# Kernel optimization log

Hardware: AMD Instinct MI355X
Metric: run time of the kernel (lower is better)

The kernel has to match this reference:

```python
import jax, jax.numpy as jnp
import numpy as np

B, S, D, H = 2, 4096, 1024, 16
HD = D // H
KCONV = 4


def _rmsnorm(x, scale, eps=1e-6):
    return x * jax.lax.rsqrt(jnp.mean(x * x, axis=-1, keepdims=True) + eps) * scale


def _l2norm(x, eps=1e-6):
    return x * jax.lax.rsqrt(jnp.sum(x * x, axis=-1, keepdims=True) + eps)


def _causal_dwconv_silu(x, w):
    # x: [B,S,D], w: [D,K] depthwise taps (tap K-1 multiplies x[t])
    k = w.shape[1]
    s = x.shape[1]
    xp = jnp.pad(x, ((0, 0), (k - 1, 0), (0, 0)))
    out = sum(xp[:, i:i + s, :] * w[:, i] for i in range(k))
    return jax.nn.silu(out)


def _p20_scan(x, decay_log, theta):
    # BLOCK_DIAGONAL_2 rotary-state linear recurrence: channels paired into
    # complex state, s_t = a * s_{t-1} + u_t with a = exp(-exp(decay_log) + i*theta).
    b, s, d = x.shape
    xc = x.reshape(b, s, d // 2, 2)
    u = jax.lax.complex(xc[..., 0], xc[..., 1])  # [B,S,D/2]
    a = jnp.exp(-jnp.exp(decay_log)) * jnp.exp(1j * theta)  # [D/2] complex, |a|<1

    def step(carry, u_t):
        st = carry * a + u_t
        return st, st

    _, ys = jax.lax.scan(step, jnp.zeros((b, d // 2), u.dtype), jnp.swapaxes(u, 0, 1))
    ys = jnp.swapaxes(ys, 0, 1)  # [B,S,D/2]
    return jnp.stack([ys.real, ys.imag], axis=-1).reshape(b, s, d)


def _gated_delta_rule(q, k, v, g, beta):
    # q,k,v: [B,S,H,Dh]; g,beta: [B,S,H]. State S: [B,H,K,V].
    scale = q.shape[-1] ** -0.5
    q = _l2norm(q)
    k = _l2norm(k)
    qt, kt, vt = (jnp.moveaxis(t, 1, 0) for t in (q, k, v))
    gt, bt = (jnp.moveaxis(t, 1, 0) for t in (g, beta))
    s0 = jnp.zeros((q.shape[0], q.shape[2], q.shape[3], v.shape[3]), v.dtype)

    def step(state, inp):
        q_t, k_t, v_t, g_t, b_t = inp
        state = state * jnp.exp(g_t)[..., None, None]
        v_err = (v_t - jnp.einsum('bhkv,bhk->bhv', state, k_t)) * b_t[..., None]
        state = state + jnp.einsum('bhk,bhv->bhkv', k_t, v_err)
        o_t = jnp.einsum('bhkv,bhk->bhv', state, q_t) * scale
        return state, o_t

    _, o = jax.lax.scan(step, s0, (qt, kt, vt, gt, bt))
    return jnp.moveaxis(o, 0, 1)  # [B,S,H,V]


def setup_inputs() -> dict:
    key = jax.random.key(0)
    ks = jax.random.split(key, 16)
    w = lambda k, shp, s=0.02: (jax.random.normal(k, shp, jnp.float32) * s)
    ctrl_out = 3 * D + 2 * H + D  # q,k,v,decay,beta,output_gate
    ctrl_b = jnp.concatenate([
        jnp.zeros((3 * D,), jnp.float32),
        jnp.full((H,), 1.5, jnp.float32),       # decay bias
        jnp.full((H,), -2.0, jnp.float32),      # beta bias
        jnp.full((D,), -1.5, jnp.float32),      # output gate bias
    ])
    # depthwise conv init: delta at last tap + small noise
    def conv_w(k):
        base = jnp.zeros((D, KCONV), jnp.float32).at[:, -1].set(1.0)
        return base + w(k, (D, KCONV), 0.02)
    return {
        'hidden': jax.random.normal(ks[0], (B, S, D), jnp.float32),
        'p20_decay_log': w(ks[1], (D // 2,), 1.0),
        'p20_theta': jax.random.uniform(ks[2], (D // 2,), jnp.float32, 0.0, 2.0 * np.pi),
        'ctrl_W': w(ks[3], (D, ctrl_out)),
        'ctrl_b': ctrl_b,
        'p20c_W': w(ks[4], (D, 3 * D), 0.001),  # 0.05-scaled init
        'qconv_w': conv_w(ks[5]),
        'kconv_w': conv_w(ks[6]),
        'vconv_w': conv_w(ks[7]),
        'mnorm_scale': jnp.ones((HD,), jnp.float32),
        'vnorm_scale': jnp.ones((D,), jnp.float32),
        'ramp_logit': jnp.full((D,), -4.595, jnp.float32),  # logit(0.01)
        'out_W': w(ks[8], (2 * D, D), 0.02),
        'out_b': jnp.zeros((D,), jnp.float32),
    }


def reference(hidden, p20_decay_log, p20_theta, ctrl_W, ctrl_b, p20c_W,
              qconv_w, kconv_w, vconv_w, mnorm_scale, vnorm_scale,
              ramp_logit, out_W, out_b):
    b, s, d = hidden.shape
    # P20 vector-state side channel
    p20_read = _p20_scan(hidden, p20_decay_log, p20_theta)
    normed_p20 = _rmsnorm(p20_read, vnorm_scale)
    p20_q, p20_k, p20_v = jnp.split(normed_p20 @ p20c_W, 3, axis=-1)
    ramp = jax.nn.sigmoid(ramp_logit)  # [D]
    # packed control projection
    ctrl = hidden @ ctrl_W + ctrl_b
    q_in, k_in, v_in, dec_in, beta_in, gate_in = jnp.split(
        ctrl, np.cumsum([d, d, d, H, H]).tolist(), axis=-1)
    # causal depthwise conv + SiLU
    q_in = _causal_dwconv_silu(q_in, qconv_w)
    k_in = _causal_dwconv_silu(k_in, kconv_w)
    v_in = _causal_dwconv_silu(v_in, vconv_w)
    # P20-conditioned heads
    queries = (q_in + ramp * p20_q).reshape(b, s, H, HD)
    keys = (k_in + ramp * p20_k).reshape(b, s, H, HD)
    values = (v_in + ramp * p20_v).reshape(b, s, H, HD)
    g = jax.nn.log_sigmoid(dec_in.astype(jnp.float32)).astype(hidden.dtype)  # [B,S,H]
    beta = jax.nn.sigmoid(beta_in)
    reads = _gated_delta_rule(queries, keys, values, g, beta)
    normed_reads = _rmsnorm(reads, mnorm_scale).reshape(b, s, d)
    fused = jnp.concatenate([normed_reads, normed_p20], axis=-1)
    projected = fused @ out_W + out_b
    return jax.nn.sigmoid(gate_in) * projected
```

## Files before the change

kernel.cpp:

```cpp
#include <hip/hip_runtime.h>
#include <hip/hip_bf16.h>
#include <stdint.h>

#define SEQ  4096
#define NH   16
#define HD   64

typedef __attribute__((ext_vector_type(8))) short bf16x8;
typedef __attribute__((ext_vector_type(4))) float f32x4;

__device__ __forceinline__ float bf2f(unsigned short u){
  union{unsigned u;float f;} v; v.u = ((unsigned)u)<<16; return v.f;
}
__device__ __forceinline__ unsigned short f2bf(float f){
  union{float f;unsigned u;} v; v.f=f;
  return (unsigned short)((v.u + 0x7fffu + ((v.u>>16)&1u))>>16);
}
__device__ __forceinline__ float sigm(float x){ return 1.f/(1.f+__expf(-x)); }
__device__ __forceinline__ f32x4 mfma16(bf16x8 a, bf16x8 b, f32x4 c){
  return __builtin_amdgcn_mfma_f32_16x16x32_bf16(a,b,c,0,0,0);
}
__device__ __forceinline__ void gll16(const void* g, void* l){
  __builtin_amdgcn_global_load_lds((const __attribute__((address_space(1))) void*)g,
                                   (__attribute__((address_space(3))) void*)l, 16, 0, 0);
}

__global__ void k_fill(float* __restrict__ p, float v, long n){
  long i = (long)blockIdx.x*blockDim.x + threadIdx.x;
  long stride = (long)gridDim.x*blockDim.x;
  for (; i<n; i+=stride) p[i] = v;
}

__global__ void k_cvt_bf16(const float* __restrict__ in, unsigned short* __restrict__ out){
  long i = ((long)blockIdx.x*256 + threadIdx.x)*4;
  float4 v = *(const float4*)(in+i);
  ushort4 o; o.x=f2bf(v.x); o.y=f2bf(v.y); o.z=f2bf(v.z); o.w=f2bf(v.w);
  *(ushort4*)(out+i) = o;
}

__global__ void k_transpose(const float* __restrict__ in, unsigned short* __restrict__ out,
                            int R, int Cin, int Cpad){
  __shared__ float t[32][33];
  int cb = blockIdx.x*32, rb = blockIdx.y*32;
  int tx = threadIdx.x & 31, ty = threadIdx.x >> 5;
  for (int k=0;k<32;k+=8){
    int r = rb+ty+k, c = cb+tx;
    t[ty+k][tx] = (c<Cin) ? in[(long)r*Cin + c] : 0.f;
  }
  __syncthreads();
  for (int k=0;k<32;k+=8){
    int c = cb+ty+k, r = rb+tx;
    if (c<Cpad) out[(long)c*R + r] = f2bf(t[tx][ty+k]);
  }
}

#define FOR16(F) F(0,0) F(0,1) F(0,2) F(0,3) F(1,0) F(1,1) F(1,2) F(1,3) \
                 F(2,0) F(2,1) F(2,2) F(2,3) F(3,0) F(3,1) F(3,2) F(3,3)
#define FOR4(F) F(0) F(1) F(2) F(3)
#define ACC(i,j) Ac##i##j

#define GEMM_CORE(A_,lda_,Bt_,ldb_,K_)                                         \
  __shared__ unsigned short Ab[3][4096];                                       \
  __shared__ unsigned short Bb[3][4096];                                       \
  const int tid=threadIdx.x, wid=tid>>6, l=tid&63;                             \
  const int nbx=(int)gridDim.x;                                               \
  const int nwg=nbx*(int)gridDim.y;                                           \
  int flat=(int)blockIdx.y*nbx+(int)blockIdx.x;                                \
  flat=(flat&7)*(nwg>>3)+(flat>>3);                                           \
  const long m0=(long)(flat/nbx)*128, n0=(long)(flat%nbx)*128;                 \
  const int nk=(K_)>>5;                                                        \
  const int wm=(wid>>1)*64, wn=(wid&1)*64;                                     \
  const int srow0 = tid>>2;                                                    \
  const int schunk = (((tid&3) ^ ((tid>>4)&3))<<3);                            \
  const unsigned short* gA0 = (A_) + (m0+srow0)*(lda_) + schunk;               \
  const unsigned short* gA1 = (A_) + (m0+64+srow0)*(lda_) + schunk;            \
  const unsigned short* gB0 = (Bt_) + (n0+srow0)*(ldb_) + schunk;              \
  const unsigned short* gB1 = (Bt_) + (n0+64+srow0)*(ldb_) + schunk;           \
  const int ldst0 = tid*16, ldst1 = 4096 + tid*16;                             \
  f32x4 Ac00={0.f,0.f,0.f,0.f};                                                \
  f32x4 Ac01=Ac00,Ac02=Ac00,Ac03=Ac00,Ac10=Ac00,Ac11=Ac00,Ac12=Ac00,           \
        Ac13=Ac00,Ac20=Ac00,Ac21=Ac00,Ac22=Ac00,Ac23=Ac00,Ac30=Ac00,           \
        Ac31=Ac00,Ac32=Ac00,Ac33=Ac00;                                         \
  gll16(gA0, (char*)&Ab[0][0]+ldst0); gll16(gA1, (char*)&Ab[0][0]+ldst1);      \
  gll16(gB0, (char*)&Bb[0][0]+ldst0); gll16(gB1, (char*)&Bb[0][0]+ldst1);      \
  gA0+=32; gA1+=32; gB0+=32; gB1+=32;                                          \
  gll16(gA0, (char*)&Ab[1][0]+ldst0); gll16(gA1, (char*)&Ab[1][0]+ldst1);      \
  gll16(gB0, (char*)&Bb[1][0]+ldst0); gll16(gB1, (char*)&Bb[1][0]+ldst1);      \
  gA0+=32; gA1+=32; gB0+=32; gB1+=32;                                          \
  int rb=0, sb=2;                                                              \
  const int sxor = ((l>>2)&3)<<4;                                              \
  const int rao0 = (wm+(l&15))*64 + (((l>>4)<<4) ^ sxor);                      \
  const int rbo0 = (wn+(l&15))*64 + (((l>>4)<<4) ^ sxor);                      \
  for (int kt=0; kt<nk; ++kt){                                                 \
    if (kt+1<nk) { asm volatile("s_waitcnt vmcnt(4)" ::: "memory"); }          \
    else         { asm volatile("s_waitcnt vmcnt(0)" ::: "memory"); }          \
    __builtin_amdgcn_sched_barrier(0);                                         \
    __builtin_amdgcn_s_barrier();                                              \
    __builtin_amdgcn_sched_barrier(0);                                         \
    if (kt+2<nk){                                                              \
      gll16(gA0, (char*)&Ab[sb][0]+ldst0); gll16(gA1, (char*)&Ab[sb][0]+ldst1);\
      gll16(gB0, (char*)&Bb[sb][0]+ldst0); gll16(gB1, (char*)&Bb[sb][0]+ldst1);\
      gA0+=32; gA1+=32; gB0+=32; gB1+=32;                                      \
    }                                                                          \
    const char* Apt=(const char*)&Ab[rb][0];                                   \
    const char* Bpt=(const char*)&Bb[rb][0];                                   \
    bf16x8 af0=*(const bf16x8*)(Apt+rao0);      bf16x8 bf0=*(const bf16x8*)(Bpt+rbo0);      \
    bf16x8 af1=*(const bf16x8*)(Apt+rao0+1024); bf16x8 bf1=*(const bf16x8*)(Bpt+rbo0+1024); \
    bf16x8 af2=*(const bf16x8*)(Apt+rao0+2048); bf16x8 bf2=*(const bf16x8*)(Bpt+rbo0+2048); \
    bf16x8 af3=*(const bf16x8*)(Apt+rao0+3072); bf16x8 bf3=*(const bf16x8*)(Bpt+rbo0+3072); \
    __builtin_amdgcn_s_setprio(1);                                             \
    Ac00=mfma16(af0,bf0,Ac00); Ac01=mfma16(af0,bf1,Ac01);                      \
    Ac02=mfma16(af0,bf2,Ac02); Ac03=mfma16(af0,bf3,Ac03);                      \
    Ac10=mfma16(af1,bf0,Ac10); Ac11=mfma16(af1,bf1,Ac11);                      \
    Ac12=mfma16(af1,bf2,Ac12); Ac13=mfma16(af1,bf3,Ac13);                      \
    Ac20=mfma16(af2,bf0,Ac20); Ac21=mfma16(af2,bf1,Ac21);                      \
    Ac22=mfma16(af2,bf2,Ac22); Ac23=mfma16(af2,bf3,Ac23);                      \
    Ac30=mfma16(af3,bf0,Ac30); Ac31=mfma16(af3,bf1,Ac31);                      \
    Ac32=mfma16(af3,bf2,Ac32); Ac33=mfma16(af3,bf3,Ac33);                      \
    __builtin_amdgcn_s_setprio(0);                                             \
    rb = (rb==2)?0:rb+1; sb = (sb==2)?0:sb+1;                                  \
  }

__global__ __launch_bounds__(256,2) void k_gemm(
  const unsigned short* __restrict__ A, int lda,
  const unsigned short* __restrict__ Bt, int ldb,
  unsigned short* Cb, float* Cf, int ldc,
  int K, int Nvalid,
  const float* __restrict__ bias,
  const unsigned short* __restrict__ gate, int gld)
{
  GEMM_CORE(A, lda, Bt, ldb, K)
#define EPI_GEN(mi,ni) {                                                       \
  const int gn=(int)n0+wn+ni*16+(l&15);                                        \
  if (gn<Nvalid){                                                              \
    _Pragma("unroll") for(int r=0;r<4;r++){                                    \
      const long gm=m0+wm+mi*16+((l>>4)<<2)+r;                                 \
      float v=ACC(mi,ni)[r];                                                   \
      if(bias) v+=bias[gn];                                                    \
      if(gate) v*=bf2f(gate[gm*gld+gn]);                                       \
      if(Cb) Cb[gm*ldc+gn]=f2bf(v); else Cf[gm*ldc+gn]=v; } } }
  FOR16(EPI_GEN)
#undef EPI_GEN
}

__global__ __launch_bounds__(256,2) void k_gemm_ctrl(
  const unsigned short* __restrict__ A, int lda,
  const unsigned short* __restrict__ Bt, int ldb,
  unsigned short* __restrict__ ctrl,
  float* __restrict__ gbuf, float* __restrict__ bbuf,
  unsigned short* __restrict__ gateb,
  const float* __restrict__ bias)
{
  GEMM_CORE(A, lda, Bt, ldb, 1024)
#define EPI_CTRL(mi,ni) {                                                      \
  const int gn=(int)n0+wn+ni*16+(l&15);                                        \
  if (gn<4128){                                                                \
    const float bs=bias[gn];                                                   \
    _Pragma("unroll") for(int r=0;r<4;r++){                                    \
      const long gm=m0+wm+mi*16+((l>>4)<<2)+r;                                 \
      float v=ACC(mi,ni)[r]+bs;                                                \
      if (gn<3072)      ctrl[gm*3072+gn]=f2bf(v);                              \
      else if (gn<3088) gbuf[gm*16+(gn-3072)]=                                 \
                          (v>=0.f)?-log1pf(__expf(-v)):(v-log1pf(__expf(v)));  \
      else if (gn<3104) bbuf[gm*16+(gn-3088)]=sigm(v);                         \
      else              gateb[gm*1024+(gn-3104)]=f2bf(sigm(v)); } } }
  FOR16(EPI_CTRL)
#undef EPI_CTRL
}

__global__ __launch_bounds__(256,2) void k_gemm_qkv(
  const unsigned short* __restrict__ A, int lda,
  const unsigned short* __restrict__ Bt, int ldb,
  const float* __restrict__ ramp,
  unsigned short* __restrict__ Qb, unsigned short* __restrict__ Kb,
  unsigned short* __restrict__ Vb)
{
  GEMM_CORE(A, lda, Bt, ldb, 1024)
  const int seg = (int)((n0 + wn) >> 10);
  unsigned short* Ob = (seg==0)?Qb:((seg==1)?Kb:Vb);
  const int dc0=((int)n0+wn+0*16+(l&15))&1023; const float sr0=sigm(ramp[dc0]);
  const int dc1=((int)n0+wn+1*16+(l&15))&1023; const float sr1=sigm(ramp[dc1]);
  const int dc2=((int)n0+wn+2*16+(l&15))&1023; const float sr2=sigm(ramp[dc2]);
  const int dc3=((int)n0+wn+3*16+(l&15))&1023; const float sr3=sigm(ramp[dc3]);
#define EPI_QKV(mi) {                                                          \
  _Pragma("unroll") for(int r=0;r<4;r++){                                      \
    const long gm=m0+wm+mi*16+((l>>4)<<2)+r;                                   \
    float v0=bf2f(Ob[gm*1024+dc0])+sr0*ACC(mi,0)[r];                           \
    float v1=bf2f(Ob[gm*1024+dc1])+sr1*ACC(mi,1)[r];                           \
    float v2=bf2f(Ob[gm*1024+dc2])+sr2*ACC(mi,2)[r];                           \
    float v3=bf2f(Ob[gm*1024+dc3])+sr3*ACC(mi,3)[r];                           \
    if (seg<2){                                                                \
      float ss=v0*v0+v1*v1+v2*v2+v3*v3;                                        \
      ss+=__shfl_xor(ss,1); ss+=__shfl_xor(ss,2);                              \
      ss+=__shfl_xor(ss,4); ss+=__shfl_xor(ss,8);                              \
      float rs=rsqrtf(ss+1e-6f); v0*=rs; v1*=rs; v2*=rs; v3*=rs; }             \
    Ob[gm*1024+dc0]=f2bf(v0); Ob[gm*1024+dc1]=f2bf(v1);                        \
    Ob[gm*1024+dc2]=f2bf(v2); Ob[gm*1024+dc3]=f2bf(v3); } }
  FOR4(EPI_QKV)
#undef EPI_QKV
}

__global__ void k_scan1(const float* __restrict__ hidden, const float* __restrict__ dlog,
                        const float* __restrict__ theta, float2* __restrict__ finals){
  int idx = blockIdx.x*256 + threadIdx.x;
  int ch = idx & 511; int chunk = (idx>>9) & 63; int b = idx>>15;
  float e = __expf(dlog[ch]); float r = __expf(-e);
  float th = theta[ch]; float ar = r*__cosf(th), ai = r*__sinf(th);
  const float2* src = (const float2*)hidden + ((long)b*SEQ + chunk*64)*512 + ch;
  float sr=0.f, si=0.f;
  for (int j=0;j<64;j++){
    float2 u = src[(long)j*512];
    float nr = sr*ar - si*ai + u.x;
    si = sr*ai + si*ar + u.y; sr = nr;
  }
  finals[idx] = make_float2(sr,si);
}
__global__ void k_scan2(const float* __restrict__ dlog, const float* __restrict__ theta,
                        const float2* __restrict__ finals, float2* __restrict__ carry, int nb){
  int idx = blockIdx.x*256+threadIdx.x; if (idx>=nb*512) return;
  int ch = idx & 511, b = idx>>9;
  float e = __expf(dlog[ch]); float r64 = __expf(-64.f*e);
  float ang = fmodf(64.f*theta[ch], 6.2831853071795864f);
  float cr = r64*__cosf(ang), ci = r64*__sinf(ang);
  float pr=0.f, pi=0.f;
  for (int c=0;c<64;c++){
    long o = ((long)b*64 + c)*512 + ch;
    carry[o] = make_float2(pr,pi);
    float2 f = finals[o];
    float nr = pr*cr - pi*ci + f.x;
    pi = pr*ci + pi*cr + f.y; pr = nr;
  }
}
__global__ void k_scan3(const float* __restrict__ hidden, const float* __restrict__ dlog,
                        const float* __restrict__ theta, const float2* __restrict__ carry,
                        unsigned short* __restrict__ p20){
  int idx = blockIdx.x*256 + threadIdx.x;
  int ch = idx & 511; int chunk = (idx>>9) & 63; int b = idx>>15;
  float e = __expf(dlog[ch]); float r = __expf(-e);
  float th = theta[ch]; float ar = r*__cosf(th), ai = r*__sinf(th);
  long toff = (long)b*SEQ + chunk*64;
  const float2* src = (const float2*)hidden + toff*512 + ch;
  unsigned short* dst = p20 + toff*1024 + 2*ch;
  float2 c0 = carry[idx];
  float sr=c0.x, si=c0.y;
  for (int j=0;j<64;j++){
    float2 u = src[(long)j*512];
    float nr = sr*ar - si*ai + u.x;
    si = sr*ai + si*ar + u.y; sr = nr;
    ushort2 o; o.x=f2bf(sr); o.y=f2bf(si);
    *(ushort2*)(dst + (long)j*1024) = o;
  }
}

__global__ __launch_bounds__(256) void k_rms_p20(const unsigned short* __restrict__ p20,
                        const float* __restrict__ vns, unsigned short* __restrict__ fused){
  long t = blockIdx.x;
  int d = threadIdx.x*4;
  ushort4 xu = *(const ushort4*)(p20 + t*1024 + d);
  float x0=bf2f(xu.x), x1=bf2f(xu.y), x2=bf2f(xu.z), x3=bf2f(xu.w);
  float ss = x0*x0 + x1*x1 + x2*x2 + x3*x3;
  for (int o=1;o<64;o<<=1) ss += __shfl_xor(ss, o);
  __shared__ float red[4];
  if ((threadIdx.x&63)==0) red[threadIdx.x>>6] = ss;
  __syncthreads();
  ss = red[0]+red[1]+red[2]+red[3];
  float rs = rsqrtf(ss*(1.f/1024.f) + 1e-6f);
  float4 s4 = *(const float4*)(vns + d);
  ushort4 o4;
  o4.x = f2bf(x0*rs*s4.x); o4.y = f2bf(x1*rs*s4.y);
  o4.z = f2bf(x2*rs*s4.z); o4.w = f2bf(x3*rs*s4.w);
  *(ushort4*)(fused + t*2048 + 1024 + d) = o4;
}

__global__ __launch_bounds__(256) void k_conv(const unsigned short* __restrict__ ctrl,
   const float* __restrict__ qw, const float* __restrict__ kw, const float* __restrict__ vw,
   unsigned short* __restrict__ Q, unsigned short* __restrict__ Kb, unsigned short* __restrict__ Vb){
  __shared__ unsigned short pan[19][256];
  int panel = blockIdx.x;
  int tb = blockIdx.y;
  int b = tb >> 8; int s0 = (tb & 255) * 16;
  int seg = panel >> 2; int d = (panel & 3)*256 + threadIdx.x;
  int c0 = panel*256;
  long base = (long)b*SEQ*3072;
  for (int rr=0; rr<19; rr++){
    int s = s0 - 3 + rr;
    pan[rr][threadIdx.x] = (s>=0) ? ctrl[base + (long)s*3072 + c0 + threadIdx.x] : (unsigned short)0;
  }
  __syncthreads();
  const float* cw = (seg==0)?qw:((seg==1)?kw:vw);
  float w0=cw[d*4], w1=cw[d*4+1], w2=cw[d*4+2], w3=cw[d*4+3];
  unsigned short* Ob = (seg==0)?Q:((seg==1)?Kb:Vb);
  for (int tk=0; tk<16; tk++){
    long t = (long)b*SEQ + s0 + tk;
    float x = bf2f(pan[tk][threadIdx.x])*w0 + bf2f(pan[tk+1][threadIdx.x])*w1
            + bf2f(pan[tk+2][threadIdx.x])*w2 + bf2f(pan[tk+3][threadIdx.x])*w3;
    x = x * sigm(x);
    Ob[t*1024 + d] = f2bf(x);
  }
}

__global__ __launch_bounds__(64,2) void k_phase1(
    const unsigned short* __restrict__ Kg, const unsigned short* __restrict__ Vg,
    const float* __restrict__ g, const float* __restrict__ beta,
    unsigned short* __restrict__ uvT, unsigned short* __restrict__ Wrm,
    unsigned short* __restrict__ Mc, unsigned short* __restrict__ BcT){
  __shared__ unsigned short Kc[64*64];
  __shared__ unsigned short Vc[64*64];
  __shared__ float Af[64*64];
  __shared__ unsigned short uTb[64*72];
  __shared__ unsigned short wTb[64*72];
  __shared__ float Gs[64], betl[64], bgam[64], decC[64];

  int bid = blockIdx.x; int bh = bid>>6, c = bid&63;
  int blocal = bh>>4, h = bh&15;
  long t0 = (long)blocal*SEQ + c*64;
  int l = threadIdx.x;
  long cbase = (long)bid*4096;

  float G = g[(t0+l)*16 + h];
  for (int o=1;o<64;o<<=1){ float n = __shfl_up(G,o); if (l>=o) G += n; }
  float bl = beta[(t0+l)*16+h];
  Gs[l]=G; betl[l]=bl; bgam[l]=bl*__expf(G);
  float G63 = __shfl(G,63);
  decC[l] = __expf(G63 - G);
  float GamC = __expf(G63);

  for (int it=0; it<8; it++){
    int bo = it*1024 + l*16;
    int row = bo>>7, bib = bo&127;
    int sb2 = bib ^ ((row&7)<<4);
    gll16(Kg + (t0+row)*1024 + h*64 + (sb2>>1),  (char*)Kc + bo);
    gll16(Vg + (t0+row)*1024 + h*64 + (bib>>1), (char*)Vc + bo);
  }
  __syncthreads();

  bf16x8 kf[2][4];
  {
    int rr = l&15;
    #pragma unroll
    for (int t=0;t<4;t++)
      #pragma unroll
      for (int h2=0;h2<2;h2++){
        int row = t*16 + rr;
        int byt = row*128 + ((h2*64 + (l>>4)*16) ^ ((row&7)<<4));
        kf[h2][t] = *(const bf16x8*)((const char*)Kc + byt);
      }
  }
  #pragma unroll
  for (int ti=0;ti<4;ti++){
    #pragma unroll
    for (int tj=0;tj<4;tj++){
      f32x4 a = {0.f,0.f,0.f,0.f};
// ... 160 lines not shown
    short4 s4 = *(const short4*)&Sst[cbase + flat];
    *(short4*)((char*)ST + v*128 + ((2*kd0) ^ ((v&7)<<4))) = s4;
  }
  __syncthreads();

  bf16x8 qf[2][4], kfr[2][4], sf[2][4];
  #pragma unroll
  for (int t=0;t<4;t++){
    long tr = t0 + t*16 + (l&15);
    qf[0][t]  = *(const bf16x8*)(Qg + tr*1024 + h*64 + (l>>4)*8);
    qf[1][t]  = *(const bf16x8*)(Qg + tr*1024 + h*64 + 32 + (l>>4)*8);
    kfr[0][t] = *(const bf16x8*)(Kg + tr*1024 + h*64 + (l>>4)*8);
    kfr[1][t] = *(const bf16x8*)(Kg + tr*1024 + h*64 + 32 + (l>>4)*8);
    int v = t*16 + (l&15);
    sf[0][t] = *(const bf16x8*)((const char*)ST + v*128 + (((l>>4)*16) ^ ((v&7)<<4)));
    sf[1][t] = *(const bf16x8*)((const char*)ST + v*128 + ((64+(l>>4)*16) ^ ((v&7)<<4)));
  }

  f32x4 qs[4][4];
  #pragma unroll
  for (int ti=0;ti<4;ti++)
    #pragma unroll
    for (int tj=0;tj<4;tj++){
      f32x4 a = {0.f,0.f,0.f,0.f};
      a = mfma16(qf[0][ti], sf[0][tj], a);
      a = mfma16(qf[1][ti], sf[1][tj], a);
      qs[ti][tj] = a;
    }

  #pragma unroll
  for (int ti=0;ti<4;ti++)
    #pragma unroll
    for (int tj=0;tj<4;tj++){
      f32x4 a = {0.f,0.f,0.f,0.f};
      a = mfma16(qf[0][ti], kfr[0][tj], a);
      a = mfma16(qf[1][ti], kfr[1][tj], a);
      int j = tj*16 + (l&15);
      float Gj = Gs[j];
      #pragma unroll
      for (int r=0;r<4;r++){
        int i = ti*16 + ((l>>4)<<2) + r;
        float v = (j<=i)? a[r]*__expf(Gs[i]-Gj) : 0.f;
        *(unsigned short*)((char*)QKl + i*128 + ((2*j) ^ ((i&7)<<4))) = f2bf(v);
      }
    }

  #pragma unroll
  for (int ti=0; ti<4; ti++){
    int irow = ti*16 + (l&15);
    bf16x8 w0 = *(const bf16x8*)(Wrm + cbase + irow*64 + (l>>4)*8);
    bf16x8 w1 = *(const bf16x8*)(Wrm + cbase + irow*64 + 32 + (l>>4)*8);
    #pragma unroll
    for (int tj=0; tj<4; tj++){
      f32x4 a = {0.f,0.f,0.f,0.f};
      a = mfma16(w0, sf[0][tj], a);
      a = mfma16(w1, sf[1][tj], a);
      int v = tj*16 + (l&15);
      int i0 = ti*16 + ((l>>4)<<2);
      short4 uv4 = *(const short4*)(uvT + cbase + (long)v*64 + i0);
      short4 p;
      p.x=(short)f2bf(bf2f((unsigned short)uv4.x) - a[0]);
      p.y=(short)f2bf(bf2f((unsigned short)uv4.y) - a[1]);
      p.z=(short)f2bf(bf2f((unsigned short)uv4.z) - a[2]);
      p.w=(short)f2bf(bf2f((unsigned short)uv4.w) - a[3]);
      *(short4*)((char*)uT + v*128 + ((2*i0) ^ ((v&7)<<4))) = p;
    }
  }
  __syncthreads();

  float mscale[4];
  #pragma unroll
  for (int tj=0;tj<4;tj++) mscale[tj] = mns[tj*16 + (l&15)];
  #pragma unroll
  for (int ti=0; ti<4; ti++){
    int row = ti*16 + (l&15);
    bf16x8 qk0 = *(const bf16x8*)((const char*)QKl + row*128 + (((l>>4)*16) ^ ((row&7)<<4)));
    bf16x8 qk1 = *(const bf16x8*)((const char*)QKl + row*128 + ((64+(l>>4)*16) ^ ((row&7)<<4)));
    #pragma unroll
    for (int tj=0; tj<4; tj++){
      int v = tj*16 + (l&15);
      bf16x8 u0 = *(const bf16x8*)((const char*)uT + v*128 + (((l>>4)*16) ^ ((v&7)<<4)));
      bf16x8 u1 = *(const bf16x8*)((const char*)uT + v*128 + ((64+(l>>4)*16) ^ ((v&7)<<4)));
      f32x4 a;
      #pragma unroll
      for (int r=0;r<4;r++){
        float gam = __expf(Gs[ti*16 + ((l>>4)<<2) + r]);
        a[r] = qs[ti][tj][r]*gam;
      }
      a = mfma16(qk0,u0,a);
      a = mfma16(qk1,u1,a);
      qs[ti][tj] = a;
    }
  }
  #pragma unroll
  for (int ti=0; ti<4; ti++){
    #pragma unroll
    for (int r=0; r<4; r++){
      float ss = 0.f;
      #pragma unroll
      for (int tj=0;tj<4;tj++){ float v = qs[ti][tj][r]*0.125f; ss += v*v; }
      ss += __shfl_xor(ss,1); ss += __shfl_xor(ss,2); ss += __shfl_xor(ss,4); ss += __shfl_xor(ss,8);
      float rs = rsqrtf(ss*(1.f/64.f) + 1e-6f);
      long t = t0 + ti*16 + ((l>>4)<<2) + r;
      #pragma unroll
      for (int tj=0;tj<4;tj++){
        float on = qs[ti][tj][r]*0.125f*rs*mscale[tj];
        fused[t*2048 + h*64 + tj*16 + (l&15)] = f2bf(on);
      }
    }
  }
}

extern "C" void kernel_launch(void* const* d_in, const int* in_sizes, int n_in,
                              void* d_out, int out_size, void* d_ws, size_t ws_size,
                              hipStream_t stream){
  (void)in_sizes; (void)n_in;
  const float* hidden = (const float*)d_in[0];
  const float* dlog   = (const float*)d_in[1];
  const float* theta  = (const float*)d_in[2];
  const float* ctrlW  = (const float*)d_in[3];
  const float* ctrlb  = (const float*)d_in[4];
  const float* p20cW  = (const float*)d_in[5];
  const float* qw     = (const float*)d_in[6];
  const float* kw     = (const float*)d_in[7];
  const float* vw     = (const float*)d_in[8];
  const float* mns    = (const float*)d_in[9];
  const float* vns    = (const float*)d_in[10];
  const float* ramp   = (const float*)d_in[11];
  const float* outW   = (const float*)d_in[12];
  const float* outb   = (const float*)d_in[13];
  float* out = (float*)d_out;

  struct Bufs {
    unsigned short *ctrl, *uvT, *Wrm, *Mc;
    unsigned short *Qb, *Kb, *Vb, *fused;
    unsigned short *E_hid, *E_p20, *BcT;
    unsigned short *Sst, *gateb, *ctrlWT, *p20WT, *outWT;
    float2 *finals, *carry; float *gbuf, *bbuf;
    size_t need;
  };
  auto mk = [&](size_t NT)->Bufs{
    Bufs B; size_t off=0;
    auto tk=[&](size_t n)->char*{ char* p=(char*)d_ws+off; off += (n+255)&~(size_t)255; return p; };
    char* Rctrl = tk(NT*3072*2);
    B.ctrl=(unsigned short*)Rctrl;
    B.uvT=(unsigned short*)Rctrl; B.Wrm=B.uvT + NT*1024; B.Mc=B.Wrm + NT*1024;
    char* Rqkv = tk(NT*1024*2*3);
    B.Qb=(unsigned short*)Rqkv; B.Kb=B.Qb+NT*1024; B.Vb=B.Kb+NT*1024;
    B.fused=(unsigned short*)tk(NT*2048*2);
    char* RE = tk(NT*1024*2);
    B.E_hid=(unsigned short*)RE; B.E_p20=(unsigned short*)RE; B.BcT=(unsigned short*)RE;
    B.Sst=(unsigned short*)tk(NT*1024*2);
    B.gateb=(unsigned short*)tk(NT*1024*2);
    B.ctrlWT=(unsigned short*)tk((size_t)4224*1024*2);
    B.p20WT=(unsigned short*)tk((size_t)3072*1024*2);
    B.outWT=(unsigned short*)tk((size_t)1024*2048*2);
    B.finals=(float2*)tk(NT*64);
    B.carry=(float2*)tk(NT*64);
    B.gbuf=(float*)tk(NT*16*4);
    B.bbuf=(float*)tk(NT*16*4);
    B.need=off;
    return B;
  };

  Bufs Bf = mk(8192);
  Bufs Bh = mk(4096);
  Bufs B; size_t NT; int nb;
  if      (Bf.need <= ws_size){ B=Bf; NT=8192; nb=2; }
  else if (Bh.need <= ws_size){ B=Bh; NT=4096; nb=1; }
  else {
    k_fill<<<2048,256,0,stream>>>(out, (float)((double)ws_size), (long)out_size);
    return;
  }

  k_transpose<<<dim3(132,32),256,0,stream>>>(ctrlW, B.ctrlWT, 1024, 4128, 4224);
  k_transpose<<<dim3(96,32), 256,0,stream>>>(p20cW, B.p20WT, 1024, 3072, 3072);
  k_transpose<<<dim3(32,64), 256,0,stream>>>(outW,  B.outWT, 2048, 1024, 1024);

  for (int b0=0; b0<2; b0+=nb){
    const float* hidb = hidden + (size_t)b0*SEQ*1024;
    float* outp = out + (size_t)b0*SEQ*1024;
    k_cvt_bf16<<<(int)NT,256,0,stream>>>(hidb, B.E_hid);
    k_gemm_ctrl<<<dim3(33,NT/128),256,0,stream>>>(B.E_hid,1024, B.ctrlWT,1024,
                                                  B.ctrl, B.gbuf, B.bbuf, B.gateb, ctrlb);
    k_scan1<<<nb*128,256,0,stream>>>(hidb,dlog,theta,B.finals);
    k_scan2<<<nb*2, 256,0,stream>>>(dlog,theta,B.finals,B.carry,nb);
    k_scan3<<<nb*128,256,0,stream>>>(hidb,dlog,theta,B.carry,B.E_p20);
    k_rms_p20<<<(int)NT,256,0,stream>>>(B.E_p20,vns,B.fused);
    k_conv<<<dim3(12,NT/16),256,0,stream>>>(B.ctrl,qw,kw,vw,B.Qb,B.Kb,B.Vb);
    k_gemm_qkv<<<dim3(24,NT/128),256,0,stream>>>(B.fused+1024,2048, B.p20WT,1024,
                                                 ramp, B.Qb,B.Kb,B.Vb);
    k_phase1<<<(int)(NT/4),64,0,stream>>>(B.Kb,B.Vb,B.gbuf,B.bbuf,B.uvT,B.Wrm,B.Mc,B.BcT);
    k_phase2<<<nb*64,64,0,stream>>>(B.Mc,B.BcT,B.Sst);
    k_phase3<<<(int)(NT/4),64,0,stream>>>(B.Qb,B.Kb,B.gbuf,B.uvT,B.Wrm,B.Sst,mns,B.fused);
    k_gemm<<<dim3(8,NT/128),256,0,stream>>>(B.fused,2048, B.outWT,2048,
                                            nullptr,outp,1024, 2048,1024, outb, B.gateb,1024);
  }
}
```

Before: 543.6 us.

## Use 256x256-tile 512-thread GEMM core for ctrl and qkv projections

Adds a new GEMM core with 256x256 output tiles, 8 waves, K-step of 64 and double-buffered LDS with staggered A/B prefetches between MFMA halves. The ctrl and qkv projection kernels move onto it, and the ctrl weight transpose is padded to 4352 columns so N tiles align to 256. Larger tiles raise arithmetic intensity and cut global traffic. In exchange the kernels use 128 KB of LDS and more accumulator registers, and the grids become small (17x32, 12x32), which may leave CUs underused. The LDS layout also drops the XOR swizzle, which may cause bank conflicts.

Measured after the change: 626.4 us. +15.2%, slower.

```diff
diff --git a/kernel.cpp b/kernel.cpp
--- a/kernel.cpp
+++ b/kernel.cpp
@@ -56,17 +56,188 @@
 
 #define FOR16(F) F(0,0) F(0,1) F(0,2) F(0,3) F(1,0) F(1,1) F(1,2) F(1,3) \
                  F(2,0) F(2,1) F(2,2) F(2,3) F(3,0) F(3,1) F(3,2) F(3,3)
-#define FOR4(F) F(0) F(1) F(2) F(3)
+#define FOR84(F) \
+ F(0,0) F(0,1) F(0,2) F(0,3) F(1,0) F(1,1) F(1,2) F(1,3) \
+ F(2,0) F(2,1) F(2,2) F(2,3) F(3,0) F(3,1) F(3,2) F(3,3) \
+ F(4,0) F(4,1) F(4,2) F(4,3) F(5,0) F(5,1) F(5,2) F(5,3) \
+ F(6,0) F(6,1) F(6,2) F(6,3) F(7,0) F(7,1) F(7,2) F(7,3)
+#define FOR8(F) F(0) F(1) F(2) F(3) F(4) F(5) F(6) F(7)
 #define ACC(i,j) Ac##i##j
-
+#define SBAR0 __builtin_amdgcn_sched_barrier(0)
+
+#define MF4(A_,B0_,B1_,B2_,B3_,C0_,C1_,C2_,C3_) \
+  C0_=mfma16(A_,B0_,C0_); C1_=mfma16(A_,B1_,C1_); \
+  C2_=mfma16(A_,B2_,C2_); C3_=mfma16(A_,B3_,C3_);
+
+#define GEMM256_CORE(A_,lda_,Bt_,ldb_,K_)                                      \
+  __shared__ unsigned short LAs[32768];        \
+  __shared__ unsigned short LBs[32768];                                        \
+  const int tid=threadIdx.x, wid=tid>>6, l=tid&63;                             \
+  const int nbx=(int)gridDim.x;                                                \
+  const int nwg=nbx*(int)gridDim.y;                                            \
+  int flat=(int)blockIdx.y*nbx+(int)blockIdx.x;                                \
+  flat=(flat&7)*(nwg>>3)+(flat>>3);                                            \
+  const long m0=(long)(flat/nbx)*256, n0=(long)(flat%nbx)*256;                 \
+  const int wr=wid>>2, wc=wid&3;                                               \
+  const int nt=(K_)>>6;                                                        \
+  char* LA=(char*)LAs; char* LB=(char*)LBs;                                    \
+  const unsigned short* pA0=(A_)+(m0+(tid>>2))*(lda_)+(tid&3)*8;               \
+  const unsigned short* pA1=pA0+128*(lda_);                                    \
+  const unsigned short* pB0=(Bt_)+(n0+(tid>>2))*(ldb_)+(tid&3)*8;              \
+  const unsigned short* pB1=pB0+128*(ldb_);                                    \
+  const int dst=tid*16;                                                        \
+  f32x4 Ac00={0.f,0.f,0.f,0.f};                                                \
+  f32x4 Ac01=Ac00,Ac02=Ac00,Ac03=Ac00,Ac10=Ac00,Ac11=Ac00,Ac12=Ac00,Ac13=Ac00, \
+        Ac20=Ac00,Ac21=Ac00,Ac22=Ac00,Ac23=Ac00,Ac30=Ac00,Ac31=Ac00,Ac32=Ac00, \
+        Ac33=Ac00,Ac40=Ac00,Ac41=Ac00,Ac42=Ac00,Ac43=Ac00,Ac50=Ac00,Ac51=Ac00, \
+        Ac52=Ac00,Ac53=Ac00,Ac60=Ac00,Ac61=Ac00,Ac62=Ac00,Ac63=Ac00,Ac70=Ac00, \
+        Ac71=Ac00,Ac72=Ac00,Ac73=Ac00;                                         \
+             \
+  gll16(pA0,    LA+dst); gll16(pA1,    LA+8192+dst);                  \
+  gll16(pB0,    LB+dst); gll16(pB1,    LB+8192+dst);                  \
+  gll16(pA0+32, LA+16384+dst); gll16(pA1+32, LA+24576+dst);           \
+  gll16(pB0+32, LB+16384+dst); gll16(pB1+32, LB+24576+dst);           \
+  const int aro=(wr*128+(l&15))*64+((l>>4)<<4);                                \
+  const int bro=(wc*64 +(l&15))*64+((l>>4)<<4);                                \
+  for (int t=0;t<nt;++t){                                                      \
+    const int buf=(t&1)*32768, nb2=32768-buf;                                  \
+    const long kn=((long)(t+1))<<6;                                            \
+    const char* Ap0=LA+buf;       const char* Bp0=LB+buf;                      \
+    const char* Ap1=Ap0+16384;    const char* Bp1=Bp0+16384;                   \
+    const bool st=(t+1<nt);                                                    \
+                                          \
+    asm volatile("s_waitcnt vmcnt(4)":::"memory");                             \
+    SBAR0; __builtin_amdgcn_s_barrier(); SBAR0;                                \
+    bf16x8 Fb0=*(const bf16x8*)(Bp0+bro);                                      \
+    bf16x8 Fb1=*(const bf16x8*)(Bp0+bro+1024);                                 \
+    bf16x8 Fb2=*(const bf16x8*)(Bp0+bro+2048);                                 \
+    bf16x8 Fb3=*(const bf16x8*)(Bp0+bro+3072);                                 \
+    bf16x8 Fa0=*(const bf16x8*)(Ap0+aro);                                      \
+    bf16x8 Fa1=*(const bf16x8*)(Ap0+aro+1024);                                 \
+    bf16x8 Fa2=*(const bf16x8*)(Ap0+aro+2048);                                 \
+    bf16x8 Fa3=*(const bf16x8*)(Ap0+aro+3072);                                 \
+    if (st){ gll16(pA0+kn, LA+nb2+dst); gll16(pA1+kn, LA+nb2+8192+dst); }      \
+    __builtin_amdgcn_s_setprio(1);                                             \
+    MF4(Fa0,Fb0,Fb1,Fb2,Fb3, Ac00,Ac01,Ac02,Ac03)                              \
+    MF4(Fa1,Fb0,Fb1,Fb2,Fb3, Ac10,Ac11,Ac12,Ac13)                              \
+    MF4(Fa2,Fb0,Fb1,Fb2,Fb3, Ac20,Ac21,Ac22,Ac23)                              \
+    MF4(Fa3,Fb0,Fb1,Fb2,Fb3, Ac30,Ac31,Ac32,Ac33)                              \
+    __builtin_amdgcn_s_setprio(0);                                             \
+    __builtin_amdgcn_s_barrier();                                              \
+                                 \
+    Fa0=*(const bf16x8*)(Ap0+aro+4096);                                        \
+    Fa1=*(const bf16x8*)(Ap0+aro+5120);                                        \
+    Fa2=*(const bf16x8*)(Ap0+aro+6144);                                        \
+    Fa3=*(const bf16x8*)(Ap0+aro+7168);                                        \
+    if (st){ gll16(pB0+kn, LB+nb2+dst); gll16(pB1+kn, LB+nb2+8192+dst); }      \
+    __builtin_amdgcn_s_setprio(1);                                             \
+    MF4(Fa0,Fb0,Fb1,Fb2,Fb3, Ac40,Ac41,Ac42,Ac43)                              \
+    MF4(Fa1,Fb0,Fb1,Fb2,Fb3, Ac50,Ac51,Ac52,Ac53)                              \
+    MF4(Fa2,Fb0,Fb1,Fb2,Fb3, Ac60,Ac61,Ac62,Ac63)                              \
+    MF4(Fa3,Fb0,Fb1,Fb2,Fb3, Ac70,Ac71,Ac72,Ac73)                              \
+    __builtin_amdgcn_s_setprio(0);                                             \
+    __builtin_amdgcn_s_barrier();                                              \
+                                          \
+    if (st){ asm volatile("s_waitcnt vmcnt(4)":::"memory"); }                  \
+    else   { asm volatile("s_waitcnt vmcnt(0)":::"memory"); }                  \
+    SBAR0; __builtin_amdgcn_s_barrier(); SBAR0;                                \
+    Fb0=*(const bf16x8*)(Bp1+bro);                                             \
+    Fb1=*(const bf16x8*)(Bp1+bro+1024);                                        \
+    Fb2=*(const bf16x8*)(Bp1+bro+2048);                                        \
+    Fb3=*(const bf16x8*)(Bp1+bro+3072);                                        \
+    Fa0=*(const bf16x8*)(Ap1+aro);                                             \
+    Fa1=*(const bf16x8*)(Ap1+aro+1024);                                        \
+    Fa2=*(const bf16x8*)(Ap1+aro+2048);                                        \
+    Fa3=*(const bf16x8*)(Ap1+aro+3072);                                        \
+    if (st){ gll16(pA0+kn+32, LA+nb2+16384+dst); gll16(pA1+kn+32, LA+nb2+24576+dst); } \
+    __builtin_amdgcn_s_setprio(1);                                             \
+    MF4(Fa0,Fb0,Fb1,Fb2,Fb3, Ac00,Ac01,Ac02,Ac03)                              \
+    MF4(Fa1,Fb0,Fb1,Fb2,Fb3, Ac10,Ac11,Ac12,Ac13)                              \
+    MF4(Fa2,Fb0,Fb1,Fb2,Fb3, Ac20,Ac21,Ac22,Ac23)                              \
+    MF4(Fa3,Fb0,Fb1,Fb2,Fb3, Ac30,Ac31,Ac32,Ac33)                              \
+    __builtin_amdgcn_s_setprio(0);                                             \
+    __builtin_amdgcn_s_barrier();                                              \
+                                 \
+    Fa0=*(const bf16x8*)(Ap1+aro+4096);                                        \
+    Fa1=*(const bf16x8*)(Ap1+aro+5120);                                        \
+    Fa2=*(const bf16x8*)(Ap1+aro+6144);                                        \
+    Fa3=*(const bf16x8*)(Ap1+aro+7168);                                        \
+    if (st){ gll16(pB0+kn+32, LB+nb2+16384+dst); gll16(pB1+kn+32, LB+nb2+24576+dst); } \
+    __builtin_amdgcn_s_setprio(1);                                             \
+    MF4(Fa0,Fb0,Fb1,Fb2,Fb3, Ac40,Ac41,Ac42,Ac43)                              \
+    MF4(Fa1,Fb0,Fb1,Fb2,Fb3, Ac50,Ac51,Ac52,Ac53)                              \
+    MF4(Fa2,Fb0,Fb1,Fb2,Fb3, Ac60,Ac61,Ac62,Ac63)                              \
+    MF4(Fa3,Fb0,Fb1,Fb2,Fb3, Ac70,Ac71,Ac72,Ac73)                              \
+    __builtin_amdgcn_s_setprio(0);                                             \
+    __builtin_amdgcn_s_barrier();                                              \
+  }
+
+__global__ __launch_bounds__(512,2) void k_gemm_ctrl(
+  const unsigned short* __restrict__ A, int lda,
+  const unsigned short* __restrict__ Bt, int ldb,
+  unsigned short* __restrict__ ctrl,
+  float* __restrict__ gbuf, float* __restrict__ bbuf,
+  unsigned short* __restrict__ gateb,
+  const float* __restrict__ bias)
+{
+  GEMM256_CORE(A, lda, Bt, ldb, 1024)
+#define EPI_CTRL(fm,fn) {                                                      \
+  const int gn=(int)n0+wc*64+fn*16+(l&15);                                     \
+  if (gn<4128){                                                                \
+    const float bs=bias[gn];                                                   \
+    _Pragma("unroll") for(int r=0;r<4;r++){                                    \
+      const long gm=m0+wr*128+fm*16+((l>>4)<<2)+r;                             \
+      float v=ACC(fm,fn)[r]+bs;                                                \
+      if (gn<3072)      ctrl[gm*3072+gn]=f2bf(v);                              \
+      else if (gn<3088) gbuf[gm*16+(gn-3072)]=                                 \
+                          (v>=0.f)?-log1pf(__expf(-v)):(v-log1pf(__expf(v)));  \
+      else if (gn<3104) bbuf[gm*16+(gn-3088)]=sigm(v);                         \
+      else              gateb[gm*1024+(gn-3104)]=f2bf(sigm(v)); } } }
+  FOR84(EPI_CTRL)
+#undef EPI_CTRL
+}
+
+__global__ __launch_bounds__(512,2) void k_gemm_qkv(
+  const unsigned short* __restrict__ A, int lda,
+  const unsigned short* __restrict__ Bt, int ldb,
+  const float* __restrict__ ramp,
+  unsigned short* __restrict__ Qb, unsigned short* __restrict__ Kb,
+  unsigned short* __restrict__ Vb)
+{
+  GEMM256_CORE(A, lda, Bt, ldb, 1024)
+  const int seg = (int)((n0 + wc*64) >> 10);
+  unsigned short* Ob = (seg==0)?Qb:((seg==1)?Kb:Vb);
+  const int dc0=((int)n0+wc*64+ 0+(l&15))&1023; const float sr0=sigm(ramp[dc0]);
+  const int dc1=((int)n0+wc*64+16+(l&15))&1023; const float sr1=sigm(ramp[dc1]);
+  const int dc2=((int)n0+wc*64+32+(l&15))&1023; const float sr2=sigm(ramp[dc2]);
+  const int dc3=((int)n0+wc*64+48+(l&15))&1023; const float sr3=sigm(ramp[dc3]);
+#define EPI_QKV(fm) {                                                          \
+  _Pragma("unroll") for(int r=0;r<4;r++){                                      \
+    const long gm=m0+wr*128+fm*16+((l>>4)<<2)+r;                               \
+    float v0=bf2f(Ob[gm*1024+dc0])+sr0*ACC(fm,0)[r];                           \
+    float v1=bf2f(Ob[gm*1024+dc1])+sr1*ACC(fm,1)[r];                           \
+    float v2=bf2f(Ob[gm*1024+dc2])+sr2*ACC(fm,2)[r];                           \
+    float v3=bf2f(Ob[gm*1024+dc3])+sr3*ACC(fm,3)[r];                           \
+    if (seg<2){                                                                \
+      float ss=v0*v0+v1*v1+v2*v2+v3*v3;                                        \
+      ss+=__shfl_xor(ss,1); ss+=__shfl_xor(ss,2);                              \
+      ss+=__shfl_xor(ss,4); ss+=__shfl_xor(ss,8);                              \
+      float rs=rsqrtf(ss+1e-6f); v0*=rs; v1*=rs; v2*=rs; v3*=rs; }             \
+    Ob[gm*1024+dc0]=f2bf(v0); Ob[gm*1024+dc1]=f2bf(v1);                        \
+    Ob[gm*1024+dc2]=f2bf(v2); Ob[gm*1024+dc3]=f2bf(v3); } }
+  FOR8(EPI_QKV)
+#undef EPI_QKV
+}
+
+#define ACC2(i,j) Bc##i##j
 #define GEMM_CORE(A_,lda_,Bt_,ldb_,K_)                                         \
   __shared__ unsigned short Ab[3][4096];                                       \
   __shared__ unsigned short Bb[3][4096];                                       \
   const int tid=threadIdx.x, wid=tid>>6, l=tid&63;                             \
-  const int nbx=(int)gridDim.x;                                               \
-  const int nwg=nbx*(int)gridDim.y;                                           \
+  const int nbx=(int)gridDim.x;                                                \
+  const int nwg=nbx*(int)gridDim.y;                                            \
   int flat=(int)blockIdx.y*nbx+(int)blockIdx.x;                                \
-  flat=(flat&7)*(nwg>>3)+(flat>>3);                                           \
+  flat=(flat&7)*(nwg>>3)+(flat>>3);                                            \
   const long m0=(long)(flat/nbx)*128, n0=(long)(flat%nbx)*128;                 \
   const int nk=(K_)>>5;                                                        \
   const int wm=(wid>>1)*64, wn=(wid&1)*64;                                     \
@@ -77,10 +248,10 @@
   const unsigned short* gB0 = (Bt_) + (n0+srow0)*(ldb_) + schunk;              \
   const unsigned short* gB1 = (Bt_) + (n0+64+srow0)*(ldb_) + schunk;           \
   const int ldst0 = tid*16, ldst1 = 4096 + tid*16;                             \
-  f32x4 Ac00={0.f,0.f,0.f,0.f};                                                \
-  f32x4 Ac01=Ac00,Ac02=Ac00,Ac03=Ac00,Ac10=Ac00,Ac11=Ac00,Ac12=Ac00,           \
-        Ac13=Ac00,Ac20=Ac00,Ac21=Ac00,Ac22=Ac00,Ac23=Ac00,Ac30=Ac00,           \
-        Ac31=Ac00,Ac32=Ac00,Ac33=Ac00;                                         \
+  f32x4 Bc00={0.f,0.f,0.f,0.f};                                                \
+  f32x4 Bc01=Bc00,Bc02=Bc00,Bc03=Bc00,Bc10=Bc00,Bc11=Bc00,Bc12=Bc00,           \
+        Bc13=Bc00,Bc20=Bc00,Bc21=Bc00,Bc22=Bc00,Bc23=Bc00,Bc30=Bc00,           \
+        Bc31=Bc00,Bc32=Bc00,Bc33=Bc00;                                         \
   gll16(gA0, (char*)&Ab[0][0]+ldst0); gll16(gA1, (char*)&Ab[0][0]+ldst1);      \
   gll16(gB0, (char*)&Bb[0][0]+ldst0); gll16(gB1, (char*)&Bb[0][0]+ldst1);      \
   gA0+=32; gA1+=32; gB0+=32; gB1+=32;                                          \
@@ -109,14 +280,14 @@
     bf16x8 af2=*(const bf16x8*)(Apt+rao0+2048); bf16x8 bf2=*(const bf16x8*)(Bpt+rbo0+2048); \
     bf16x8 af3=*(const bf16x8*)(Apt+rao0+3072); bf16x8 bf3=*(const bf16x8*)(Bpt+rbo0+3072); \
     __builtin_amdgcn_s_setprio(1);                                             \
-    Ac00=mfma16(af0,bf0,Ac00); Ac01=mfma16(af0,bf1,Ac01);                      \
-    Ac02=mfma16(af0,bf2,Ac02); Ac03=mfma16(af0,bf3,Ac03);                      \
-    Ac10=mfma16(af1,bf0,Ac10); Ac11=mfma16(af1,bf1,Ac11);                      \
-    Ac12=mfma16(af1,bf2,Ac12); Ac13=mfma16(af1,bf3,Ac13);                      \
-    Ac20=mfma16(af2,bf0,Ac20); Ac21=mfma16(af2,bf1,Ac21);                      \
-    Ac22=mfma16(af2,bf2,Ac22); Ac23=mfma16(af2,bf3,Ac23);                      \
-    Ac30=mfma16(af3,bf0,Ac30); Ac31=mfma16(af3,bf1,Ac31);                      \
-    Ac32=mfma16(af3,bf2,Ac32); Ac33=mfma16(af3,bf3,Ac33);                      \
+    Bc00=mfma16(af0,bf0,Bc00); Bc01=mfma16(af0,bf1,Bc01);                      \
+    Bc02=mfma16(af0,bf2,Bc02); Bc03=mfma16(af0,bf3,Bc03);                      \
+    Bc10=mfma16(af1,bf0,Bc10); Bc11=mfma16(af1,bf1,Bc11);                      \
+    Bc12=mfma16(af1,bf2,Bc12); Bc13=mfma16(af1,bf3,Bc13);                      \
+    Bc20=mfma16(af2,bf0,Bc20); Bc21=mfma16(af2,bf1,Bc21);                      \
+    Bc22=mfma16(af2,bf2,Bc22); Bc23=mfma16(af2,bf3,Bc23);                      \
+    Bc30=mfma16(af3,bf0,Bc30); Bc31=mfma16(af3,bf1,Bc31);                      \
+    Bc32=mfma16(af3,bf2,Bc32); Bc33=mfma16(af3,bf3,Bc33);                      \
     __builtin_amdgcn_s_setprio(0);                                             \
     rb = (rb==2)?0:rb+1; sb = (sb==2)?0:sb+1;                                  \
   }
@@ -135,69 +306,12 @@
   if (gn<Nvalid){                                                              \
     _Pragma("unroll") for(int r=0;r<4;r++){                                    \
       const long gm=m0+wm+mi*16+((l>>4)<<2)+r;                                 \
-      float v=ACC(mi,ni)[r];                                                   \
+      float v=ACC2(mi,ni)[r];                                                  \
       if(bias) v+=bias[gn];                                                    \
       if(gate) v*=bf2f(gate[gm*gld+gn]);                                       \
       if(Cb) Cb[gm*ldc+gn]=f2bf(v); else Cf[gm*ldc+gn]=v; } } }
   FOR16(EPI_GEN)
 #undef EPI_GEN
-}
-
-__global__ __launch_bounds__(256,2) void k_gemm_ctrl(
-  const unsigned short* __restrict__ A, int lda,
-  const unsigned short* __restrict__ Bt, int ldb,
-  unsigned short* __restrict__ ctrl,
-  float* __restrict__ gbuf, float* __restrict__ bbuf,
-  unsigned short* __restrict__ gateb,
-  const float* __restrict__ bias)
-{
-  GEMM_CORE(A, lda, Bt, ldb, 1024)
-#define EPI_CTRL(mi,ni) {                                                      \
-  const int gn=(int)n0+wn+ni*16+(l&15);                                        \
-  if (gn<4128){                                                                \
-    const float bs=bias[gn];                                                   \
-    _Pragma("unroll") for(int r=0;r<4;r++){                                    \
-      const long gm=m0+wm+mi*16+((l>>4)<<2)+r;                                 \
-      float v=ACC(mi,ni)[r]+bs;                                                \
-      if (gn<3072)      ctrl[gm*3072+gn]=f2bf(v);                              \
-      else if (gn<3088) gbuf[gm*16+(gn-3072)]=                                 \
-                          (v>=0.f)?-log1pf(__expf(-v)):(v-log1pf(__expf(v)));  \
-      else if (gn<3104) bbuf[gm*16+(gn-3088)]=sigm(v);                         \
-      else              gateb[gm*1024+(gn-3104)]=f2bf(sigm(v)); } } }
-  FOR16(EPI_CTRL)
-#undef EPI_CTRL
-}
-
-__global__ __launch_bounds__(256,2) void k_gemm_qkv(
-  const unsigned short* __restrict__ A, int lda,
-  const unsigned short* __restrict__ Bt, int ldb,
-  const float* __restrict__ ramp,
-  unsigned short* __restrict__ Qb, unsigned short* __restrict__ Kb,
-  unsigned short* __restrict__ Vb)
-{
-  GEMM_CORE(A, lda, Bt, ldb, 1024)
-  const int seg = (int)((n0 + wn) >> 10);
-  unsigned short* Ob = (seg==0)?Qb:((seg==1)?Kb:Vb);
-  const int dc0=((int)n0+wn+0*16+(l&15))&1023; const float sr0=sigm(ramp[dc0]);
-  const int dc1=((int)n0+wn+1*16+(l&15))&1023; const float sr1=sigm(ramp[dc1]);
-  const int dc2=((int)n0+wn+2*16+(l&15))&1023; const float sr2=sigm(ramp[dc2]);
-  const int dc3=((int)n0+wn+3*16+(l&15))&1023; const float sr3=sigm(ramp[dc3]);
-#define EPI_QKV(mi) {                                                          \
-  _Pragma("unroll") for(int r=0;r<4;r++){                                      \
-    const long gm=m0+wm+mi*16+((l>>4)<<2)+r;                                   \
-    float v0=bf2f(Ob[gm*1024+dc0])+sr0*ACC(mi,0)[r];                           \
-    float v1=bf2f(Ob[gm*1024+dc1])+sr1*ACC(mi,1)[r];                           \
-    float v2=bf2f(Ob[gm*1024+dc2])+sr2*ACC(mi,2)[r];                           \
-    float v3=bf2f(Ob[gm*1024+dc3])+sr3*ACC(mi,3)[r];                           \
-    if (seg<2){                                                                \
-      float ss=v0*v0+v1*v1+v2*v2+v3*v3;                                        \
-      ss+=__shfl_xor(ss,1); ss+=__shfl_xor(ss,2);                              \
-      ss+=__shfl_xor(ss,4); ss+=__shfl_xor(ss,8);                              \
-      float rs=rsqrtf(ss+1e-6f); v0*=rs; v1*=rs; v2*=rs; v3*=rs; }             \
-    Ob[gm*1024+dc0]=f2bf(v0); Ob[gm*1024+dc1]=f2bf(v1);                        \
-    Ob[gm*1024+dc2]=f2bf(v2); Ob[gm*1024+dc3]=f2bf(v3); } }
-  FOR4(EPI_QKV)
-#undef EPI_QKV
 }
 
 __global__ void k_scan1(const float* __restrict__ hidden, const float* __restrict__ dlog,
@@ -664,7 +778,7 @@
     B.E_hid=(unsigned short*)RE; B.E_p20=(unsigned short*)RE; B.BcT=(unsigned short*)RE;
     B.Sst=(unsigned short*)tk(NT*1024*2);
     B.gateb=(unsigned short*)tk(NT*1024*2);
-    B.ctrlWT=(unsigned short*)tk((size_t)4224*1024*2);
+    B.ctrlWT=(unsigned short*)tk((size_t)4352*1024*2);
     B.p20WT=(unsigned short*)tk((size_t)3072*1024*2);
     B.outWT=(unsigned short*)tk((size_t)1024*2048*2);
     B.finals=(float2*)tk(NT*64);
@@ -685,7 +799,7 @@
     return;
   }
 
-  k_transpose<<<dim3(132,32),256,0,stream>>>(ctrlW, B.ctrlWT, 1024, 4128, 4224);
+  k_transpose<<<dim3(136,32),256,0,stream>>>(ctrlW, B.ctrlWT, 1024, 4128, 4352);
   k_transpose<<<dim3(96,32), 256,0,stream>>>(p20cW, B.p20WT, 1024, 3072, 3072);
   k_transpose<<<dim3(32,64), 256,0,stream>>>(outW,  B.outWT, 2048, 1024, 1024);
 
@@ -693,14 +807,14 @@
     const float* hidb = hidden + (size_t)b0*SEQ*1024;
     float* outp = out + (size_t)b0*SEQ*1024;
     k_cvt_bf16<<<(int)NT,256,0,stream>>>(hidb, B.E_hid);
-    k_gemm_ctrl<<<dim3(33,NT/128),256,0,stream>>>(B.E_hid,1024, B.ctrlWT,1024,
+    k_gemm_ctrl<<<dim3(17,NT/256),512,0,stream>>>(B.E_hid,1024, B.ctrlWT,1024,
                                                   B.ctrl, B.gbuf, B.bbuf, B.gateb, ctrlb);
     k_scan1<<<nb*128,256,0,stream>>>(hidb,dlog,theta,B.finals);
     k_scan2<<<nb*2, 256,0,stream>>>(dlog,theta,B.finals,B.carry,nb);
     k_scan3<<<nb*128,256,0,stream>>>(hidb,dlog,theta,B.carry,B.E_p20);
     k_rms_p20<<<(int)NT,256,0,stream>>>(B.E_p20,vns,B.fused);
     k_conv<<<dim3(12,NT/16),256,0,stream>>>(B.ctrl,qw,kw,vw,B.Qb,B.Kb,B.Vb);
-    k_gemm_qkv<<<dim3(24,NT/128),256,0,stream>>>(B.fused+1024,2048, B.p20WT,1024,
+    k_gemm_qkv<<<dim3(12,NT/256),512,0,stream>>>(B.fused+1024,2048, B.p20WT,1024,
                                                  ramp, B.Qb,B.Kb,B.Vb);
     k_phase1<<<(int)(NT/4),64,0,stream>>>(B.Kb,B.Vb,B.gbuf,B.bbuf,B.uvT,B.Wrm,B.Mc,B.BcT);
     k_phase2<<<nb*64,64,0,stream>>>(B.Mc,B.BcT,B.Sst);
```
